# Optimization experiments

Hardware: AMD Instinct MI355X
Metric: run time of the kernel (lower is better)

Reference implementation:

```python
import jax, jax.numpy as jnp
import numpy as np

N, E, G = 50000, 800000, 128
H, NUM_RBF, CUTOFF, TIME_DIM, L = 128, 32, 6.0, 64, 4
MAX_Z, LIGAND_NODE = 128, 1
M_IN = 3 * H + NUM_RBF + 1


def _ln(x, g, b, eps=1e-5):
    mu = x.mean(-1, keepdims=True)
    var = ((x - mu) ** 2).mean(-1, keepdims=True)
    return (x - mu) * jax.lax.rsqrt(var + eps) * g + b


def _sin_emb(t, dim):
    half = dim // 2
    freqs = jnp.exp(jnp.arange(half, dtype=jnp.float32) * (-np.log(10000.0) / (half - 1)))
    args = t[:, None] * freqs[None, :]
    return jnp.concatenate([jnp.sin(args), jnp.cos(args)], axis=-1)


def setup_inputs() -> dict:
    key = jax.random.key(0)
    ks = jax.random.split(key, 32)
    d = {}
    d['z'] = jax.random.randint(ks[0], (N,), 0, MAX_Z)
    d['node_type'] = jax.random.randint(ks[1], (N,), 0, 2)
    d['pos'] = jax.random.normal(ks[2], (N, 3), jnp.float32) * 3.0
    d['edge_index'] = jax.random.randint(ks[3], (2, E), 0, N)
    d['edge_type'] = jax.random.randint(ks[4], (E,), 0, 2)
    d['batch'] = jnp.sort(jax.random.randint(ks[5], (N,), 0, G))
    d['t'] = jax.random.uniform(ks[6], (G,), jnp.float32)

    def lin(k, fi, fo):
        return jax.random.normal(k, (fi, fo), jnp.float32) / np.sqrt(fi)

    d['emb_z'] = jax.random.normal(ks[7], (MAX_Z, H), jnp.float32) * 0.02
    d['emb_nt'] = jax.random.normal(ks[8], (2, H), jnp.float32) * 0.02
    d['in_norm_g'] = jnp.ones((H,), jnp.float32)
    d['in_norm_b'] = jnp.zeros((H,), jnp.float32)
    d['time_w1'] = lin(ks[9], TIME_DIM, H); d['time_b1'] = jnp.zeros((H,), jnp.float32)
    d['time_w2'] = lin(ks[10], H, H); d['time_b2'] = jnp.zeros((H,), jnp.float32)
    d['l_edge_emb'] = jax.random.normal(ks[11], (L, 2, H), jnp.float32) * 0.02
    d['l_msg_w1'] = jax.random.normal(ks[12], (L, M_IN, H), jnp.float32) / np.sqrt(M_IN)
    d['l_msg_b1'] = jnp.zeros((L, H), jnp.float32)
    d['l_msg_w2'] = jax.random.normal(ks[13], (L, H, H), jnp.float32) / np.sqrt(H)
    d['l_msg_b2'] = jnp.zeros((L, H), jnp.float32)
    d['l_upd_w1'] = jax.random.normal(ks[14], (L, 2 * H, H), jnp.float32) / np.sqrt(2 * H)
    d['l_upd_b1'] = jnp.zeros((L, H), jnp.float32)
    d['l_upd_w2'] = jax.random.normal(ks[15], (L, H, H), jnp.float32) / np.sqrt(H)
    d['l_upd_b2'] = jnp.zeros((L, H), jnp.float32)
    d['l_norm_g'] = jnp.ones((L, H), jnp.float32)
    d['l_norm_b'] = jnp.zeros((L, H), jnp.float32)
    d['head_w1'] = lin(ks[16], H, H); d['head_b1'] = jnp.zeros((H,), jnp.float32)
    d['head_w2'] = lin(ks[17], H, 1); d['head_b2'] = jnp.zeros((1,), jnp.float32)
    return d


def reference(z, node_type, pos, edge_index, edge_type, batch, t,
              emb_z, emb_nt, in_norm_g, in_norm_b,
              time_w1, time_b1, time_w2, time_b2,
              l_edge_emb, l_msg_w1, l_msg_b1, l_msg_w2, l_msg_b2,
              l_upd_w1, l_upd_b1, l_upd_w2, l_upd_b2, l_norm_g, l_norm_b,
              head_w1, head_b1, head_w2, head_b2):
    centers = jnp.linspace(0.0, CUTOFF, NUM_RBF)
    step = CUTOFF / (NUM_RBF - 1)
    gamma = 1.0 / max(step * step, 1e-6)

    h = emb_z[jnp.clip(z, 0, MAX_Z - 1)] + emb_nt[node_type]
    tf = jax.nn.silu(_sin_emb(t, TIME_DIM) @ time_w1 + time_b1) @ time_w2 + time_b2
    h = h + tf[batch]
    h = _ln(h, in_norm_g, in_norm_b)

    src, dst = edge_index[0], edge_index[1]
    rel = pos[src] - pos[dst]                     # [E,3]
    dist = jnp.linalg.norm(rel, axis=-1)          # [E]
    radial = jnp.exp(-gamma * (dist[:, None] - centers[None, :]) ** 2)  # [E,R]
    lig = node_type == LIGAND_NODE

    for i in range(L):
        ek = l_edge_emb[i][edge_type]             # [E,H]
        m_in = jnp.concatenate([h[src], h[dst], ek, radial, dist[:, None]], axis=-1)
        msg = jax.nn.silu(m_in @ l_msg_w1[i] + l_msg_b1[i])
        msg = jax.nn.silu(msg @ l_msg_w2[i] + l_msg_b2[i])
        sums = jax.ops.segment_sum(msg, dst, num_segments=N)
        cnt = jax.ops.segment_sum(jnp.ones((E,), h.dtype), dst, num_segments=N)
        agg = sums / jnp.clip(cnt, 1.0)[:, None]
        upd = jax.nn.silu(jnp.concatenate([h, agg], axis=-1) @ l_upd_w1[i] + l_upd_b1[i])
        upd = upd @ l_upd_w2[i] + l_upd_b2[i]
        h = jnp.where(lig[:, None], _ln(h + upd, l_norm_g[i], l_norm_b[i]), h)

    mask = lig.astype(h.dtype)
    gsum = jax.ops.segment_sum(h * mask[:, None], batch, num_segments=G)
    gcnt = jax.ops.segment_sum(mask, batch, num_segments=G)
    gf = gsum / jnp.clip(gcnt, 1.0)[:, None]
    out = jax.nn.silu(gf @ head_w1 + head_b1) @ head_w2 + head_b2
    return out.squeeze(-1)
```

## Files before the change

### kernel.cpp

```cpp
#include <hip/hip_runtime.h>
#include <hip/hip_bf16.h>

#define NN 50000
#define EE 800000
#define GG 128
#define HH 128

typedef __bf16 bf16;
typedef __attribute__((ext_vector_type(8))) __bf16 bf16x8;
typedef __attribute__((ext_vector_type(4))) float f32x4;

__device__ __forceinline__ float silu_f(float x) { return x / (1.0f + __expf(-x)); }

__global__ void prep_weights(const float* __restrict__ w1, const float* __restrict__ w2,
                             const float* __restrict__ u1, const float* __restrict__ u2,
                             const float* __restrict__ ee, const float* __restrict__ mb1,
                             bf16* __restrict__ W1abt, bf16* __restrict__ W1rt,
                             bf16* __restrict__ W2t, bf16* __restrict__ U1t,
                             bf16* __restrict__ U2t) {
    int idx = blockIdx.x * 256 + threadIdx.x;
    if (idx < 131072) {
        int l = idx >> 15, rem = idx & 32767;
        int c = rem >> 7, k = rem & 127;
        int krow = k + ((c >= 128) ? 128 : 0);
        W1abt[idx] = (bf16)w1[(size_t)l * 417 * 128 + (size_t)krow * 128 + (c & 127)];
    } else if ((idx -= 131072) < 32768) {
        int l = idx >> 13, rem = idx & 8191;
        int c = rem >> 6, k = rem & 63;
        const float* w1l = w1 + (size_t)l * 417 * 128;
        float v = 0.0f;
        if (k < 32) v = w1l[(size_t)(384 + k) * 128 + c];
        else if (k == 32) v = w1l[(size_t)416 * 128 + c];
        else if (k == 33) {
            v = mb1[l * 128 + c];
            for (int t = 0; t < 128; ++t)
                v += ee[(size_t)l * 256 + t] * w1l[(size_t)(256 + t) * 128 + c];
        } else if (k == 34) {
            for (int t = 0; t < 128; ++t)
                v += (ee[(size_t)l * 256 + 128 + t] - ee[(size_t)l * 256 + t]) *
                     w1l[(size_t)(256 + t) * 128 + c];
        }
        W1rt[idx] = (bf16)v;
    } else if ((idx -= 32768) < 65536) {
        int l = idx / 16384, rem = idx % 16384;
        int n = rem / 128, k = rem % 128;
        W2t[idx] = (bf16)w2[(size_t)l * 16384 + (size_t)k * 128 + n];
    } else if ((idx -= 65536) < 131072) {
        int l = idx / 32768, rem = idx % 32768;
        int n = rem / 256, k = rem % 256;
        U1t[idx] = (bf16)u1[(size_t)l * 32768 + (size_t)k * 128 + n];
    } else if ((idx -= 131072) < 65536) {
        int l = idx / 16384, rem = idx % 16384;
        int n = rem / 128, k = rem % 128;
        U2t[idx] = (bf16)u2[(size_t)l * 16384 + (size_t)k * 128 + n];
    }
}

__global__ void time_mlp(const float* __restrict__ t, const float* __restrict__ w1,
                         const float* __restrict__ b1, const float* __restrict__ w2,
                         const float* __restrict__ b2, float* __restrict__ tf) {
    int g = blockIdx.x, c = threadIdx.x;
    __shared__ float sL[64], uT[128];
    float tv = t[g];
    if (c < 32) {
        float fr = expf(-(float)c * (logf(10000.0f) / 31.0f));
        float arg = tv * fr;
        sL[c] = sinf(arg);
        sL[c + 32] = cosf(arg);
    }
    __syncthreads();
    float acc = b1[c];
    for (int k = 0; k < 64; ++k) acc += sL[k] * w1[k * 128 + c];
    uT[c] = silu_f(acc);
    __syncthreads();
    float acc2 = b2[c];
    for (int k = 0; k < 128; ++k) acc2 += uT[k] * w2[k * 128 + c];
    tf[g * 128 + c] = acc2;
}

__global__ void node_init(const int* __restrict__ z, const int* __restrict__ nt,
                          const int* __restrict__ batch, const float* __restrict__ tf,
                          const float* __restrict__ emb_z, const float* __restrict__ emb_nt,
                          const float* __restrict__ g, const float* __restrict__ b,
                          float* __restrict__ hg, bf16* __restrict__ hb) {
    int n = blockIdx.x, c = threadIdx.x;
    __shared__ float red[128];
    int zz = min(max(z[n], 0), 127);
    float v = emb_z[zz * 128 + c] + emb_nt[nt[n] * 128 + c] + tf[batch[n] * 128 + c];
    red[c] = v;
    __syncthreads();
    for (int s = 64; s > 0; s >>= 1) { if (c < s) red[c] += red[c + s]; __syncthreads(); }
    float mu = red[0] * (1.0f / 128.0f);
    __syncthreads();
    float dv = v - mu;
    red[c] = dv * dv;
    __syncthreads();
    for (int s = 64; s > 0; s >>= 1) { if (c < s) red[c] += red[c + s]; __syncthreads(); }
    float var = red[0] * (1.0f / 128.0f);
    float o = dv * rsqrtf(var + 1e-5f) * g[c] + b[c];
    hg[(size_t)n * 128 + c] = o;
    hb[(size_t)n * 128 + c] = (bf16)o;
}

__global__ void edge_pre(const int* __restrict__ ei, const float* __restrict__ pos,
                         float* __restrict__ dist_raw, int* __restrict__ cnt) {
    int e = blockIdx.x * 256 + threadIdx.x;
    if (e >= EE) return;
    int s = ei[e], d = ei[EE + e];
    float dx = pos[s * 3 + 0] - pos[d * 3 + 0];
    float dy = pos[s * 3 + 1] - pos[d * 3 + 1];
    float dz = pos[s * 3 + 2] - pos[d * 3 + 2];
    dist_raw[e] = sqrtf(dx * dx + dy * dy + dz * dz);
    atomicAdd(&cnt[d], 1);
}

__global__ void scan_kernel(const int* __restrict__ cnt, int* __restrict__ cursor) {
    __shared__ int part[1024];
    int t = threadIdx.x;
    const int per = (NN + 1023) / 1024;
    int start = t * per, end = min(start + per, NN);
    int s = 0;
    for (int i = start; i < end; ++i) s += cnt[i];
    part[t] = s;
    __syncthreads();
    for (int off = 1; off < 1024; off <<= 1) {
        int v = (t >= off) ? part[t - off] : 0;
        __syncthreads();
        part[t] += v;
        __syncthreads();
    }
    int base = (t == 0) ? 0 : part[t - 1];
    for (int i = start; i < end; ++i) { cursor[i] = base; base += cnt[i]; }
}

__global__ void scatter_kernel(const int* __restrict__ ei, const int* __restrict__ et,
                               const float* __restrict__ dist_raw, int* __restrict__ cursor,
                               int* __restrict__ src_s, int* __restrict__ dst_s,
                               int* __restrict__ type_s, float* __restrict__ dist_s) {
    int e = blockIdx.x * 256 + threadIdx.x;
    if (e >= EE) return;
    int d = ei[EE + e];
    int p = atomicAdd(&cursor[d], 1);
    src_s[p] = ei[e];
    dst_s[p] = d;
    type_s[p] = et[e];
    dist_s[p] = dist_raw[e];
}

__global__ __launch_bounds__(256) void node_pre(
    const bf16* __restrict__ hb, const bf16* __restrict__ W1abt,
    bf16* __restrict__ Xsb, bf16* __restrict__ Xdb) {
    __shared__ bf16 xL[64 * 128];
    const int tid = threadIdx.x;
    const int lane = tid & 63, wave = tid >> 6;
    const int wr = wave >> 1, wc = wave & 1;
    const int lrow = lane & 15, lgrp = lane >> 4;
    const int nb0 = blockIdx.x * 64;
    const int r0 = wr * 32 + lrow, r1 = r0 + 16;

    for (int i = tid; i < 64 * 16; i += 256) {
        const int row = i >> 4, cc = i & 15;
        const int node = nb0 + row;
        bf16x8 v;
        if (node < NN) v = *(const bf16x8*)(hb + (size_t)node * 128 + cc * 8);
        else { for (int j = 0; j < 8; ++j) v[j] = (bf16)0.0f; }
        *(bf16x8*)(xL + row * 128 + ((cc ^ (row & 15)) * 8)) = v;
    }
    __syncthreads();

    f32x4 acc[2][8] = {};
    for (int ks = 0; ks < 4; ++ks) {
        const int cb = ks * 4 + lgrp;
        bf16x8 a0 = *(const bf16x8*)(xL + r0 * 128 + ((cb ^ (r0 & 15)) * 8));
        bf16x8 a1 = *(const bf16x8*)(xL + r1 * 128 + ((cb ^ (r1 & 15)) * 8));
        const int k0 = ks * 32 + lgrp * 8;
#pragma unroll
        for (int ni = 0; ni < 8; ++ni) {
            const int col = wc * 128 + ni * 16 + lrow;
            bf16x8 b = *(const bf16x8*)(W1abt + (size_t)col * 128 + k0);
            acc[0][ni] = __builtin_amdgcn_mfma_f32_16x16x32_bf16(a0, b, acc[0][ni], 0, 0, 0);
            acc[1][ni] = __builtin_amdgcn_mfma_f32_16x16x32_bf16(a1, b, acc[1][ni], 0, 0, 0);
        }
    }
#pragma unroll
    for (int mi = 0; mi < 2; ++mi) {
#pragma unroll
        for (int r = 0; r < 4; ++r) {
            const int row = wr * 32 + mi * 16 + lgrp * 4 + r;
            const int node = nb0 + row;
            if (node >= NN) continue;
#pragma unroll
            for (int ni = 0; ni < 8; ++ni) {
                const int col = wc * 128 + ni * 16 + lrow;
                float v = (mi == 0 ? acc[0][ni][r] : acc[1][ni][r]);
                if (col < 128) Xsb[(size_t)node * 128 + col] = (bf16)v;
                else Xdb[(size_t)node * 128 + (col - 128)] = (bf16)v;
            }
        }
    }
}

__global__ __launch_bounds__(256) void edge_kernel(
    const int* __restrict__ src_s, const int* __restrict__ dst_s,
    const int* __restrict__ type_s, const float* __restrict__ dist_s,
    const bf16* __restrict__ Xsb, const bf16* __restrict__ Xdb,
    const bf16* __restrict__ W1rt, const bf16* __restrict__ W2t,
    const float* __restrict__ b2, float* __restrict__ sums) {
    __shared__ bf16 xsL[64 * 128];
    __shared__ bf16 xdL[64 * 128];
    __shared__ int dstL[64];
    __shared__ int srcL[64];
    const int tid = threadIdx.x;
    const int lane = tid & 63, wave = tid >> 6;
    const int wr = wave >> 1, wc = wave & 1;
    const int lrow = lane & 15, lgrp = lane >> 4;
    const int eb = blockIdx.x * 64;

    const int r0 = wr * 32 + lrow;
    const int r1 = r0 + 16;
    const int e0 = eb + r0, e1 = eb + r1;
    const int ty0 = type_s[e0], ty1 = type_s[e1];
    const float di0 = dist_s[e0], di1 = dist_s[e1];
    if (tid < 64) { dstL[tid] = dst_s[eb + tid]; srcL[tid] = src_s[eb + tid]; }
    __syncthreads();

#pragma unroll
    for (int it = 0; it < 4; ++it) {
        const int ci = tid + it * 256;
        const int row = ci >> 4, cc = ci & 15;
        const int ccs = (cc ^ (row & 15)) << 3;
        bf16x8 vs = *(const bf16x8*)(Xsb + (size_t)srcL[row] * 128 + ccs);
        bf16x8 vd = *(const bf16x8*)(Xdb + (size_t)dstL[row] * 128 + ccs);
        *(bf16x8*)(xsL + ci * 8) = vs;
        *(bf16x8*)(xdL + ci * 8) = vd;
    }

    const float step = 6.0f / 31.0f;
    const float gamma = 1.0f / (step * step);

    f32x4 acc[2][4] = {};
#pragma unroll
    for (int ks = 0; ks < 2; ++ks) {
        const int k0 = ks * 32 + lgrp * 8;
        bf16x8 a0, a1;
        if (k0 < 32) {
#pragma unroll
            for (int j = 0; j < 8; ++j) {
                float cj = (float)(k0 + j) * step;
                float v0 = di0 - cj, v1 = di1 - cj;
                a0[j] = (bf16)__expf(-gamma * v0 * v0);
                a1[j] = (bf16)__expf(-gamma * v1 * v1);
            }
        } else {
#pragma unroll
            for (int j = 0; j < 8; ++j) { a0[j] = (bf16)0.0f; a1[j] = (bf16)0.0f; }
            if (k0 == 32) {
                a0[0] = (bf16)di0; a1[0] = (bf16)di1;
                a0[1] = (bf16)1.0f; a1[1] = (bf16)1.0f;
                a0[2] = (bf16)(float)ty0; a1[2] = (bf16)(float)ty1;
            }
        }
#pragma unroll
        for (int ni = 0; ni < 4; ++ni) {
            const int col = wc * 64 + ni * 16 + lrow;
            bf16x8 b = *(const bf16x8*)(W1rt + (size_t)col * 64 + k0);
            acc[0][ni] = __builtin_amdgcn_mfma_f32_16x16x32_bf16(a0, b, acc[0][ni], 0, 0, 0);
            acc[1][ni] = __builtin_amdgcn_mfma_f32_16x16x32_bf16(a1, b, acc[1][ni], 0, 0, 0);
        }
    }
    __syncthreads();

#pragma unroll
    for (int mi = 0; mi < 2; ++mi) {
#pragma unroll
        for (int r = 0; r < 4; ++r) {
            const int row = wr * 32 + mi * 16 + lgrp * 4 + r;
            const int base = row * 128, sw = row & 15;
#pragma unroll
            for (int ni = 0; ni < 4; ++ni) {
                const int col = wc * 64 + ni * 16 + lrow;
                const int idx = base + (((col >> 3) ^ sw) << 3) + (col & 7);
                float v = (mi == 0 ? acc[0][ni][r] : acc[1][ni][r]) +
                          (float)xsL[idx] + (float)xdL[idx];
                if (mi == 0) acc[0][ni][r] = silu_f(v);
                else acc[1][ni][r] = silu_f(v);
            }
        }
    }
    __syncthreads();

#pragma unroll
    for (int mi = 0; mi < 2; ++mi) {
#pragma unroll
        for (int r = 0; r < 4; ++r) {
            const int row = wr * 32 + mi * 16 + lgrp * 4 + r;
            const int base = row * 128, sw = row & 15;
#pragma unroll
            for (int ni = 0; ni < 4; ++ni) {
                const int col = wc * 64 + ni * 16 + lrow;
                const int idx = base + (((col >> 3) ^ sw) << 3) + (col & 7);
                xsL[idx] = (bf16)(mi == 0 ? acc[0][ni][r] : acc[1][ni][r]);
            }
        }
    }
    __syncthreads();

    f32x4 acc2[2][4] = {};
#pragma unroll
    for (int ks = 0; ks < 4; ++ks) {
        const int cb = ks * 4 + lgrp;
        bf16x8 a0 = *(const bf16x8*)(xsL + r0 * 128 + ((cb ^ (r0 & 15)) * 8));
        bf16x8 a1 = *(const bf16x8*)(xsL + r1 * 128 + ((cb ^ (r1 & 15)) * 8));
        const int k0 = ks * 32 + lgrp * 8;
#pragma unroll
        for (int ni = 0; ni < 4; ++ni) {
            const int col = wc * 64 + ni * 16 + lrow;
            bf16x8 b = *(const bf16x8*)(W2t + (size_t)col * 128 + k0);
            acc2[0][ni] = __builtin_amdgcn_mfma_f32_16x16x32_bf16(a0, b, acc2[0][ni], 0, 0, 0);
            acc2[1][ni] = __builtin_amdgcn_mfma_f32_16x16x32_bf16(a1, b, acc2[1][ni], 0, 0, 0);
        }
    }
#pragma unroll
    for (int mi = 0; mi < 2; ++mi) {
#pragma unroll
        for (int ni = 0; ni < 4; ++ni) {
            const int col = wc * 64 + ni * 16 + lrow;
            const float bias = b2[col];
#pragma unroll
            for (int r = 0; r < 4; ++r) {
                const int row = wr * 32 + mi * 16 + lgrp * 4 + r;
                float v = silu_f((mi == 0 ? acc2[0][ni][r] : acc2[1][ni][r]) + bias);
                xdL[row * 128 + col] = (bf16)v;
            }
        }
    }
    __syncthreads();
    {
        const int cp = (tid & 63) * 2;
        const int q = tid >> 6;
        float a0s = 0.0f, a1s = 0.0f;
        int cur = dstL[q * 16];
        for (int i = 0; i < 16; ++i) {
            const int row = q * 16 + i;
            const int dd = dstL[row];
            if (dd != cur) {
                atomicAdd(&sums[(size_t)cur * 128 + cp], a0s);
                atomicAdd(&sums[(size_t)cur * 128 + cp + 1], a1s);
                a0s = 0.0f; a1s = 0.0f; cur = dd;
            }
            const unsigned u = *(const unsigned*)(xdL + row * 128 + cp);
            a0s += __uint_as_float(u << 16);
            a1s += __uint_as_float(u & 0xffff0000u);
        }
        atomicAdd(&sums[(size_t)cur * 128 + cp], a0s);
        atomicAdd(&sums[(size_t)cur * 128 + cp + 1], a1s);
    }
}

__global__ __launch_bounds__(256) void node_kernel(
    float* __restrict__ hg, bf16* __restrict__ hb, float* __restrict__ sums,
    const int* __restrict__ cnt, const int* __restrict__ node_type,
    const bf16* __restrict__ U1t, const bf16* __restrict__ U2t,
    const float* __restrict__ ub1, const float* __restrict__ ub2,
    const float* __restrict__ ng, const float* __restrict__ nb_) {
    __shared__ char smem[49152];
    bf16* xL = (bf16*)smem;
    bf16* uL = (bf16*)(smem + 32768);
    float* u2f = (float*)smem;
    const int tid = threadIdx.x;
    const int lane = tid & 63, wave = tid >> 6;
    const int wr = wave >> 1, wc = wave & 1;
    const int lrow = lane & 15, lgrp = lane >> 4;
    const int nb0 = blockIdx.x * 64;
    const int r0 = wr * 32 + lrow, r1 = r0 + 16;

    for (int i = tid; i < 64 * 32; i += 256) {
        const int row = i >> 5, cc = i & 31;
        const int node = nb0 + row;
        bf16x8 v;
        if (node < NN) {
            const int col8 = cc * 8;
            if (col8 < 128) {
                v = *(const bf16x8*)(hb + (size_t)node * 128 + col8);
            } else {
                const float inv = 1.0f / fmaxf((float)cnt[node], 1.0f);
                float4* p0 = (float4*)(sums + (size_t)node * 128 + (col8 - 128));
                float4* p1 = (float4*)(sums + (size_t)node * 128 + (col8 - 128) + 4);
                const float4 f0 = *p0;
                const float4 f1 = *p1;
                v[0] = (bf16)(f0.x * inv); v[1] = (bf16)(f0.y * inv);
                v[2] = (bf16)(f0.z * inv); v[3] = (bf16)(f0.w * inv);
                v[4] = (bf16)(f1.x * inv); v[5] = (bf16)(f1.y * inv);
                v[6] = (bf16)(f1.z * inv); v[7] = (bf16)(f1.w * inv);
                *p0 = make_float4(0.f, 0.f, 0.f, 0.f);
                *p1 = make_float4(0.f, 0.f, 0.f, 0.f);
            }
        } else {
#pragma unroll
            for (int j = 0; j < 8; ++j) v[j] = (bf16)0.0f;
        }
        *(bf16x8*)(xL + row * 256 + ((cc ^ (row & 15)) * 8)) = v;
    }
    __syncthreads();

    f32x4 acc[2][4] = {};
    for (int ks = 0; ks < 8; ++ks) {
        const int cb = ks * 4 + lgrp;
        bf16x8 a0 = *(const bf16x8*)(xL + r0 * 256 + ((cb ^ (r0 & 15)) * 8));
        bf16x8 a1 = *(const bf16x8*)(xL + r1 * 256 + ((cb ^ (r1 & 15)) * 8));
        const int k0 = ks * 32 + lgrp * 8;
#pragma unroll
        for (int ni = 0; ni < 4; ++ni) {
            const int col = wc * 64 + ni * 16 + lrow;
            bf16x8 b = *(const bf16x8*)(U1t + (size_t)col * 256 + k0);
            acc[0][ni] = __builtin_amdgcn_mfma_f32_16x16x32_bf16(a0, b, acc[0][ni], 0, 0, 0);
            acc[1][ni] = __builtin_amdgcn_mfma_f32_16x16x32_bf16(a1, b, acc[1][ni], 0, 0, 0);
        }
    }
#pragma unroll
    for (int mi = 0; mi < 2; ++mi) {
#pragma unroll
        for (int ni = 0; ni < 4; ++ni) {
            const int col = wc * 64 + ni * 16 + lrow;
            const float bias = ub1[col];
            const int cc = col >> 3;
#pragma unroll
            for (int r = 0; r < 4; ++r) {
                const int row = wr * 32 + mi * 16 + lgrp * 4 + r;
                float v = silu_f((mi == 0 ? acc[0][ni][r] : acc[1][ni][r]) + bias);
                uL[row * 128 + ((cc ^ (row & 15)) * 8) + (col & 7)] = (bf16)v;
            }
        }
    }
    __syncthreads();

    f32x4 acc2[2][4] = {};
    for (int ks = 0; ks < 4; ++ks) {
        const int cb = ks * 4 + lgrp;
        bf16x8 a0 = *(const bf16x8*)(uL + r0 * 128 + ((cb ^ (r0 & 15)) * 8));
        bf16x8 a1 = *(const bf16x8*)(uL + r1 * 128 + ((cb ^ (r1 & 15)) * 8));
        const int k0 = ks * 32 + lgrp * 8;
#pragma unroll
        for (int ni = 0; ni < 4; ++ni) {
            const int col = wc * 64 + ni * 16 + lrow;
            bf16x8 b = *(const bf16x8*)(U2t + (size_t)col * 128 + k0);
            acc2[0][ni] = __builtin_amdgcn_mfma_f32_16x16x32_bf16(a0, b, acc2[0][ni], 0, 0, 0);
            acc2[1][ni] = __builtin_amdgcn_mfma_f32_16x16x32_bf16(a1, b, acc2[1][ni], 0, 0, 0);
        }
    }
    __syncthreads();
#pragma unroll
    for (int mi = 0; mi < 2; ++mi) {
#pragma unroll
        for (int ni = 0; ni < 4; ++ni) {
            const int col = wc * 64 + ni * 16 + lrow;
            const float bias = ub2[col];
#pragma unroll
            for (int r = 0; r < 4; ++r) {
                const int row = wr * 32 + mi * 16 + lgrp * 4 + r;
                u2f[row * 129 + col] = (mi == 0 ? acc2[0][ni][r] : acc2[1][ni][r]) + bias;
            }
        }
    }
    __syncthreads();
    {
        const int row = tid >> 2, sl = tid & 3;
        const int node = nb0 + row;
        const bool lig = (node < NN) && (node_type[node] == 1);
        float sum = 0.0f, sq = 0.0f;
        if (lig) {
#pragma unroll
            for (int k = 0; k < 32; ++k) {
                const int c = sl + (k << 2);
                float s = hg[(size_t)node * 128 + c] + u2f[row * 129 + c];
                u2f[row * 129 + c] = s;
                sum += s; sq += s * s;
            }
        }
        sum += __shfl_xor(sum, 1); sq += __shfl_xor(sq, 1);
        sum += __shfl_xor(sum, 2); sq += __shfl_xor(sq, 2);
        if (lig) {
            const float mu = sum * (1.0f / 128.0f);
            const float var = sq * (1.0f / 128.0f) - mu * mu;
            const float rstd = rsqrtf(var + 1e-5f);
#pragma unroll
            for (int k = 0; k < 32; ++k) {
                const int c = sl + (k << 2);
                float s = u2f[row * 129 + c];
                float o = (s - mu) * rstd * ng[c] + nb_[c];
                hg[(size_t)node * 128 + c] = o;
                hb[(size_t)node * 128 + c] = (bf16)o;
            }
        }
    }
}

__global__ void pool_kernel(const int* __restrict__ nt, const int* __restrict__ batch,
                            const float* __restrict__ hg, float* __restrict__ gsum,
                            float* __restrict__ gcnt) {
    int idx = blockIdx.x * 256 + threadIdx.x;
    int n = idx >> 7, c = idx & 127;
    if (n >= NN) return;
    if (nt[n] == 1) {
        int b = batch[n];
        atomicAdd(&gsum[b * 128 + c], hg[(size_t)n * 128 + c]);
        if (c == 0) atomicAdd(&gcnt[b], 1.0f);
    }
}

__global__ void head_kernel(const float* __restrict__ gsum, const float* __restrict__ gcnt,
                            const float* __restrict__ w1, const float* __restrict__ b1,
                            const float* __restrict__ w2, const float* __restrict__ b2,
                            float* __restrict__ out) {
    int g = blockIdx.x, c = threadIdx.x;
    __shared__ float gfL[128], uH[128];
    float inv = 1.0f / fmaxf(gcnt[g], 1.0f);
    gfL[c] = gsum[g * 128 + c] * inv;
    __syncthreads();
    float acc = b1[c];
    for (int k = 0; k < 128; ++k) acc += gfL[k] * w1[k * 128 + c];
    uH[c] = silu_f(acc);
    __syncthreads();
    gfL[c] = uH[c] * w2[c];
    __syncthreads();
    for (int s = 64; s > 0; s >>= 1) { if (c < s) gfL[c] += gfL[c + s]; __syncthreads(); }
    if (c == 0) out[g] = gfL[0] + b2[0];
}

extern "C" void kernel_launch(void* const* d_in, const int* in_sizes, int n_in,
                              void* d_out, int out_size, void* d_ws, size_t ws_size,
                              hipStream_t stream) {
    const int* z = (const int*)d_in[0];
    const int* node_type = (const int*)d_in[1];
    const float* pos = (const float*)d_in[2];
    const int* edge_index = (const int*)d_in[3];
    const int* edge_type = (const int*)d_in[4];
    const int* batch = (const int*)d_in[5];
    const float* t_in = (const float*)d_in[6];
    const float* emb_z = (const float*)d_in[7];
    const float* emb_nt = (const float*)d_in[8];
    const float* in_norm_g = (const float*)d_in[9];
    const float* in_norm_b = (const float*)d_in[10];
    const float* time_w1 = (const float*)d_in[11];
    const float* time_b1 = (const float*)d_in[12];
    const float* time_w2 = (const float*)d_in[13];
    const float* time_b2 = (const float*)d_in[14];
    const float* l_edge_emb = (const float*)d_in[15];
    const float* l_msg_w1 = (const float*)d_in[16];
    const float* l_msg_b1 = (const float*)d_in[17];
    const float* l_msg_w2 = (const float*)d_in[18];
    const float* l_msg_b2 = (const float*)d_in[19];
    const float* l_upd_w1 = (const float*)d_in[20];
    const float* l_upd_b1 = (const float*)d_in[21];
    const float* l_upd_w2 = (const float*)d_in[22];
    const float* l_upd_b2 = (const float*)d_in[23];
    const float* l_norm_g = (const float*)d_in[24];
    const float* l_norm_b = (const float*)d_in[25];
    const float* head_w1 = (const float*)d_in[26];
    const float* head_b1 = (const float*)d_in[27];
    const float* head_w2 = (const float*)d_in[28];
    const float* head_b2 = (const float*)d_in[29];
    float* out = (float*)d_out;

    char* w = (char*)d_ws;
    auto alloc = [&](size_t bytes) {
        char* p = w;
        w += (bytes + 255) & ~(size_t)255;
        return p;
    };
    float* hg = (float*)alloc((size_t)NN * 128 * 4);
    bf16* hb = (bf16*)alloc((size_t)NN * 128 * 2);
    float* sums = (float*)alloc((size_t)NN * 128 * 4);
    bf16* Xsb = (bf16*)alloc((size_t)NN * 128 * 2);
    bf16* Xdb = (bf16*)alloc((size_t)NN * 128 * 2);
    int* cnt = (int*)alloc((size_t)NN * 4);
    int* cursor = (int*)alloc((size_t)NN * 4);
    int* src_s = (int*)alloc((size_t)EE * 4);
    int* dst_s = (int*)alloc((size_t)EE * 4);
    int* type_s = (int*)alloc((size_t)EE * 4);
    float* dist_s = (float*)alloc((size_t)EE * 4);
    float* dist_raw = (float*)alloc((size_t)EE * 4);
    bf16* W1abt = (bf16*)alloc((size_t)4 * 256 * 128 * 2);
    bf16* W1rt = (bf16*)alloc((size_t)4 * 128 * 64 * 2);
    bf16* W2t = (bf16*)alloc((size_t)4 * 128 * 128 * 2);
    bf16* U1t = (bf16*)alloc((size_t)4 * 128 * 256 * 2);
    bf16* U2t = (bf16*)alloc((size_t)4 * 128 * 128 * 2);
    float* tf = (float*)alloc((size_t)GG * 128 * 4);
    float* gsum = (float*)alloc((size_t)GG * 128 * 4);
    float* gcnt = (float*)alloc((size_t)GG * 4);

    hipMemsetAsync(cnt, 0, (size_t)NN * 4, stream);
    hipMemsetAsync(sums, 0, (size_t)NN * 128 * 4, stream);
    prep_weights<<<1664, 256, 0, stream>>>(l_msg_w1, l_msg_w2, l_upd_w1, l_upd_w2,
                                           l_edge_emb, l_msg_b1, W1abt, W1rt, W2t, U1t, U2t);
    time_mlp<<<GG, 128, 0, stream>>>(t_in, time_w1, time_b1, time_w2, time_b2, tf);
    node_init<<<NN, 128, 0, stream>>>(z, node_type, batch, tf, emb_z, emb_nt,
                                      in_norm_g, in_norm_b, hg, hb);
    edge_pre<<<(EE + 255) / 256, 256, 0, stream>>>(edge_index, pos, dist_raw, cnt);
    scan_kernel<<<1, 1024, 0, stream>>>(cnt, cursor);
    scatter_kernel<<<(EE + 255) / 256, 256, 0, stream>>>(edge_index, edge_type, dist_raw,
                                                         cursor, src_s, dst_s, type_s, dist_s);
    for (int l = 0; l < 4; ++l) {
        node_pre<<<(NN + 63) / 64, 256, 0, stream>>>(hb, W1abt + (size_t)l * 32768, Xsb, Xdb);
        edge_kernel<<<EE / 64, 256, 0, stream>>>(
            src_s, dst_s, type_s, dist_s, Xsb, Xdb, W1rt + (size_t)l * 8192,
            W2t + (size_t)l * 16384, l_msg_b2 + l * 128, sums);
        node_kernel<<<(NN + 63) / 64, 256, 0, stream>>>(
            hg, hb, sums, cnt, node_type, U1t + (size_t)l * 32768, U2t + (size_t)l * 16384,
            l_upd_b1 + l * 128, l_upd_b2 + l * 128, l_norm_g + l * 128, l_norm_b + l * 128);
    }
    hipMemsetAsync(gsum, 0, (size_t)GG * 128 * 4, stream);
    hipMemsetAsync(gcnt, 0, (size_t)GG * 4, stream);
    pool_kernel<<<(NN * 128 + 255) / 256, 256, 0, stream>>>(node_type, batch, hg, gsum, gcnt);
    head_kernel<<<GG, 128, 0, stream>>>(gsum, gcnt, head_w1, head_b1, head_w2, head_b2, out);
}
```

Measured before the change: 1.603 ms.

## Transpose edge MFMA operands and gather node features directly into registers

Swaps the MFMA operand roles so weights are the A operand and per-edge activations the B operand, which puts each lane's outputs along contiguous columns of one edge. With that layout, the src/dst node feature rows are read from global memory straight into registers as 4-wide vectors instead of being staged through two shared-memory tiles. This removes one LDS buffer and several barriers, and uses a padded stride for the final message tile. In exchange the global gathers become smaller 8-byte accesses issued after the first GEMM rather than overlapped with it.

Result: no change. 1.629 ms (+1.6%).

```diff
diff --git a/kernel.cpp b/kernel.cpp
--- a/kernel.cpp
+++ b/kernel.cpp
@@ -5,9 +5,11 @@
 #define EE 800000
 #define GG 128
 #define HH 128
+#define MP 136
 
 typedef __bf16 bf16;
 typedef __attribute__((ext_vector_type(8))) __bf16 bf16x8;
+typedef __attribute__((ext_vector_type(4))) __bf16 bf16x4;
 typedef __attribute__((ext_vector_type(4))) float f32x4;
 
 __device__ __forceinline__ float silu_f(float x) { return x / (1.0f + __expf(-x)); }
@@ -206,135 +208,128 @@
     const bf16* __restrict__ Xsb, const bf16* __restrict__ Xdb,
     const bf16* __restrict__ W1rt, const bf16* __restrict__ W2t,
     const float* __restrict__ b2, float* __restrict__ sums) {
-    __shared__ bf16 xsL[64 * 128];
-    __shared__ bf16 xdL[64 * 128];
-    __shared__ int dstL[64];
-    __shared__ int srcL[64];
+    __shared__ bf16 mL[64 * MP];
+    __shared__ int srcL[64], dstL[64], typeL[64];
+    __shared__ float distL[64];
     const int tid = threadIdx.x;
     const int lane = tid & 63, wave = tid >> 6;
-    const int wr = wave >> 1, wc = wave & 1;
-    const int lrow = lane & 15, lgrp = lane >> 4;
+    const int wh = wave >> 1, wc = wave & 1;
+    const int e15 = lane & 15, lgrp = lane >> 4;
     const int eb = blockIdx.x * 64;
 
-    const int r0 = wr * 32 + lrow;
-    const int r1 = r0 + 16;
-    const int e0 = eb + r0, e1 = eb + r1;
-    const int ty0 = type_s[e0], ty1 = type_s[e1];
-    const float di0 = dist_s[e0], di1 = dist_s[e1];
-    if (tid < 64) { dstL[tid] = dst_s[eb + tid]; srcL[tid] = src_s[eb + tid]; }
-    __syncthreads();
-
-#pragma unroll
-    for (int it = 0; it < 4; ++it) {
-        const int ci = tid + it * 256;
-        const int row = ci >> 4, cc = ci & 15;
-        const int ccs = (cc ^ (row & 15)) << 3;
-        bf16x8 vs = *(const bf16x8*)(Xsb + (size_t)srcL[row] * 128 + ccs);
-        bf16x8 vd = *(const bf16x8*)(Xdb + (size_t)dstL[row] * 128 + ccs);
-        *(bf16x8*)(xsL + ci * 8) = vs;
-        *(bf16x8*)(xdL + ci * 8) = vd;
-    }
+    if (tid < 64) {
+        srcL[tid] = src_s[eb + tid];
+        dstL[tid] = dst_s[eb + tid];
+        typeL[tid] = type_s[eb + tid];
+        distL[tid] = dist_s[eb + tid];
+    }
+    __syncthreads();
+
+    const int el0 = wh * 32 + e15, el1 = el0 + 16;
+    const float d0 = distL[el0], d1 = distL[el1];
+    const float t0 = (float)typeL[el0], t1 = (float)typeL[el1];
 
     const float step = 6.0f / 31.0f;
     const float gamma = 1.0f / (step * step);
 
     f32x4 acc[2][4] = {};
-#pragma unroll
-    for (int ks = 0; ks < 2; ++ks) {
+    {
+        bf16x8 b0, b1;
+#pragma unroll
+        for (int j = 0; j < 8; ++j) {
+            float cj = (float)(lgrp * 8 + j) * step;
+            float v0 = d0 - cj, v1 = d1 - cj;
+            b0[j] = (bf16)__expf(-gamma * v0 * v0);
+            b1[j] = (bf16)__expf(-gamma * v1 * v1);
+        }
+#pragma unroll
+        for (int ct = 0; ct < 4; ++ct) {
+            const int col = wc * 64 + ct * 16 + e15;
+            bf16x8 a = *(const bf16x8*)(W1rt + (size_t)col * 64 + lgrp * 8);
+            acc[0][ct] = __builtin_amdgcn_mfma_f32_16x16x32_bf16(a, b0, acc[0][ct], 0, 0, 0);
+            acc[1][ct] = __builtin_amdgcn_mfma_f32_16x16x32_bf16(a, b1, acc[1][ct], 0, 0, 0);
+        }
+    }
+    {
+        bf16x8 b0, b1;
+#pragma unroll
+        for (int j = 0; j < 8; ++j) { b0[j] = (bf16)0.0f; b1[j] = (bf16)0.0f; }
+        if (lgrp == 0) {
+            b0[0] = (bf16)d0; b1[0] = (bf16)d1;
+            b0[1] = (bf16)1.0f; b1[1] = (bf16)1.0f;
+            b0[2] = (bf16)t0; b1[2] = (bf16)t1;
+        }
+#pragma unroll
+        for (int ct = 0; ct < 4; ++ct) {
+            const int col = wc * 64 + ct * 16 + e15;
+            bf16x8 a = *(const bf16x8*)(W1rt + (size_t)col * 64 + 32 + lgrp * 8);
+            acc[0][ct] = __builtin_amdgcn_mfma_f32_16x16x32_bf16(a, b0, acc[0][ct], 0, 0, 0);
+            acc[1][ct] = __builtin_amdgcn_mfma_f32_16x16x32_bf16(a, b1, acc[1][ct], 0, 0, 0);
+        }
+    }
+
+#pragma unroll
+    for (int et = 0; et < 2; ++et) {
+        const int eloc = wh * 32 + et * 16 + e15;
+        const bf16* xsp = Xsb + (size_t)srcL[eloc] * 128;
+        const bf16* xdp = Xdb + (size_t)dstL[eloc] * 128;
+        bf16x4 xs[4], xd[4];
+#pragma unroll
+        for (int ct = 0; ct < 4; ++ct) {
+            const int col0 = wc * 64 + ct * 16 + lgrp * 4;
+            xs[ct] = *(const bf16x4*)(xsp + col0);
+            xd[ct] = *(const bf16x4*)(xdp + col0);
+        }
+#pragma unroll
+        for (int ct = 0; ct < 4; ++ct) {
+            const int col0 = wc * 64 + ct * 16 + lgrp * 4;
+            bf16x4 pk;
+#pragma unroll
+            for (int r = 0; r < 4; ++r) {
+                float v = (et == 0 ? acc[0][ct][r] : acc[1][ct][r]) +
+                          (float)xs[ct][r] + (float)xd[ct][r];
+                pk[r] = (bf16)silu_f(v);
+            }
+            const int cc = col0 >> 3;
+            *(bf16x4*)(mL + eloc * 128 + ((cc ^ (eloc & 15)) << 3) + (col0 & 7)) = pk;
+        }
+    }
+    __syncthreads();
+
+    f32x4 acc2[2][4] = {};
+#pragma unroll
+    for (int ks = 0; ks < 4; ++ks) {
         const int k0 = ks * 32 + lgrp * 8;
-        bf16x8 a0, a1;
-        if (k0 < 32) {
-#pragma unroll
-            for (int j = 0; j < 8; ++j) {
-                float cj = (float)(k0 + j) * step;
-                float v0 = di0 - cj, v1 = di1 - cj;
-                a0[j] = (bf16)__expf(-gamma * v0 * v0);
-                a1[j] = (bf16)__expf(-gamma * v1 * v1);
-            }
-        } else {
-#pragma unroll
-            for (int j = 0; j < 8; ++j) { a0[j] = (bf16)0.0f; a1[j] = (bf16)0.0f; }
-            if (k0 == 32) {
-                a0[0] = (bf16)di0; a1[0] = (bf16)di1;
-                a0[1] = (bf16)1.0f; a1[1] = (bf16)1.0f;
-                a0[2] = (bf16)(float)ty0; a1[2] = (bf16)(float)ty1;
-            }
-        }
-#pragma unroll
-        for (int ni = 0; ni < 4; ++ni) {
-            const int col = wc * 64 + ni * 16 + lrow;
-            bf16x8 b = *(const bf16x8*)(W1rt + (size_t)col * 64 + k0);
-            acc[0][ni] = __builtin_amdgcn_mfma_f32_16x16x32_bf16(a0, b, acc[0][ni], 0, 0, 0);
-            acc[1][ni] = __builtin_amdgcn_mfma_f32_16x16x32_bf16(a1, b, acc[1][ni], 0, 0, 0);
-        }
-    }
-    __syncthreads();
-
-#pragma unroll
-    for (int mi = 0; mi < 2; ++mi) {
-#pragma unroll
-        for (int r = 0; r < 4; ++r) {
-            const int row = wr * 32 + mi * 16 + lgrp * 4 + r;
-            const int base = row * 128, sw = row & 15;
-#pragma unroll
-            for (int ni = 0; ni < 4; ++ni) {
-                const int col = wc * 64 + ni * 16 + lrow;
-                const int idx = base + (((col >> 3) ^ sw) << 3) + (col & 7);
-                float v = (mi == 0 ? acc[0][ni][r] : acc[1][ni][r]) +
-                          (float)xsL[idx] + (float)xdL[idx];
-                if (mi == 0) acc[0][ni][r] = silu_f(v);
-                else acc[1][ni][r] = silu_f(v);
-            }
-        }
-    }
-    __syncthreads();
-
-#pragma unroll
-    for (int mi = 0; mi < 2; ++mi) {
-#pragma unroll
-        for (int r = 0; r < 4; ++r) {
-            const int row = wr * 32 + mi * 16 + lgrp * 4 + r;
-            const int base = row * 128, sw = row & 15;
-#pragma unroll
-            for (int ni = 0; ni < 4; ++ni) {
-                const int col = wc * 64 + ni * 16 + lrow;
-                const int idx = base + (((col >> 3) ^ sw) << 3) + (col & 7);
-                xsL[idx] = (bf16)(mi == 0 ? acc[0][ni][r] : acc[1][ni][r]);
-            }
-        }
-    }
-    __syncthreads();
-
-    f32x4 acc2[2][4] = {};
-#pragma unroll
-    for (int ks = 0; ks < 4; ++ks) {
-        const int cb = ks * 4 + lgrp;
-        bf16x8 a0 = *(const bf16x8*)(xsL + r0 * 128 + ((cb ^ (r0 & 15)) * 8));
-        bf16x8 a1 = *(const bf16x8*)(xsL + r1 * 128 + ((cb ^ (r1 & 15)) * 8));
-        const int k0 = ks * 32 + lgrp * 8;
-#pragma unroll
-        for (int ni = 0; ni < 4; ++ni) {
-            const int col = wc * 64 + ni * 16 + lrow;
-            bf16x8 b = *(const bf16x8*)(W2t + (size_t)col * 128 + k0);
-            acc2[0][ni] = __builtin_amdgcn_mfma_f32_16x16x32_bf16(a0, b, acc2[0][ni], 0, 0, 0);
-            acc2[1][ni] = __builtin_amdgcn_mfma_f32_16x16x32_bf16(a1, b, acc2[1][ni], 0, 0, 0);
-        }
-    }
-#pragma unroll
-    for (int mi = 0; mi < 2; ++mi) {
-#pragma unroll
-        for (int ni = 0; ni < 4; ++ni) {
-            const int col = wc * 64 + ni * 16 + lrow;
-            const float bias = b2[col];
-#pragma unroll
-            for (int r = 0; r < 4; ++r) {
-                const int row = wr * 32 + mi * 16 + lgrp * 4 + r;
-                float v = silu_f((mi == 0 ? acc2[0][ni][r] : acc2[1][ni][r]) + bias);
-                xdL[row * 128 + col] = (bf16)v;
-            }
-        }
-    }
-    __syncthreads();
+        const int kc = k0 >> 3;
+        bf16x8 b0 = *(const bf16x8*)(mL + el0 * 128 + ((kc ^ (el0 & 15)) << 3));
+        bf16x8 b1 = *(const bf16x8*)(mL + el1 * 128 + ((kc ^ (el1 & 15)) << 3));
+#pragma unroll
+        for (int ct = 0; ct < 4; ++ct) {
+            const int c2 = wc * 64 + ct * 16 + e15;
+            bf16x8 a = *(const bf16x8*)(W2t + (size_t)c2 * 128 + k0);
+            acc2[0][ct] = __builtin_amdgcn_mfma_f32_16x16x32_bf16(a, b0, acc2[0][ct], 0, 0, 0);
+            acc2[1][ct] = __builtin_amdgcn_mfma_f32_16x16x32_bf16(a, b1, acc2[1][ct], 0, 0, 0);
+        }
+    }
+    __syncthreads();
+
+#pragma unroll
+    for (int et = 0; et < 2; ++et) {
+        const int eloc = wh * 32 + et * 16 + e15;
+#pragma unroll
+        for (int ct = 0; ct < 4; ++ct) {
+            const int col0 = wc * 64 + ct * 16 + lgrp * 4;
+            const float4 bb = *(const float4*)(b2 + col0);
+            bf16x4 pk;
+            pk[0] = (bf16)silu_f((et == 0 ? acc2[0][ct][0] : acc2[1][ct][0]) + bb.x);
+            pk[1] = (bf16)silu_f((et == 0 ? acc2[0][ct][1] : acc2[1][ct][1]) + bb.y);
+            pk[2] = (bf16)silu_f((et == 0 ? acc2[0][ct][2] : acc2[1][ct][2]) + bb.z);
+            pk[3] = (bf16)silu_f((et == 0 ? acc2[0][ct][3] : acc2[1][ct][3]) + bb.w);
+            *(bf16x4*)(mL + eloc * MP + col0) = pk;
+        }
+    }
+    __syncthreads();
+
     {
         const int cp = (tid & 63) * 2;
         const int q = tid >> 6;
@@ -348,7 +343,7 @@
                 atomicAdd(&sums[(size_t)cur * 128 + cp + 1], a1s);
                 a0s = 0.0f; a1s = 0.0f; cur = dd;
             }
-            const unsigned u = *(const unsigned*)(xdL + row * 128 + cp);
+            const unsigned u = *(const unsigned*)(mL + row * MP + cp);
             a0s += __uint_as_float(u << 16);
             a1s += __uint_as_float(u & 0xffff0000u);
         }
```

## Fuse next-layer node projection into node kernel and pre-sum gathered features

Applied to the files above, without the earlier changes.

The per-layer node_pre launch is folded into the tail of node_kernel, which now stages the updated bf16 node features in shared memory and computes the next layer's source/destination projections with MFMA. This removes one launch and a re-read of hb per layer. The edge kernel also adds the gathered Xs and Xd rows once while loading, storing a single padded buffer and writing silu output straight to a separate message buffer, which drops one shared-memory pass and a barrier. The trade-offs are an extra bf16 rounding of the summed projections and more shared memory and registers in node_kernel.

Result: faster. 1.387 ms (-13.5%).

```diff
diff --git a/kernel.cpp b/kernel.cpp
--- a/kernel.cpp
+++ b/kernel.cpp
@@ -5,6 +5,7 @@
 #define EE 800000
 #define GG 128
 #define HH 128
+#define XPB 136
 
 typedef __bf16 bf16;
 typedef __attribute__((ext_vector_type(8))) __bf16 bf16x8;
@@ -206,8 +207,8 @@
     const bf16* __restrict__ Xsb, const bf16* __restrict__ Xdb,
     const bf16* __restrict__ W1rt, const bf16* __restrict__ W2t,
     const float* __restrict__ b2, float* __restrict__ sums) {
-    __shared__ bf16 xsL[64 * 128];
-    __shared__ bf16 xdL[64 * 128];
+    __shared__ bf16 xbL[64 * XPB];
+    __shared__ bf16 msgL[64 * 128];
     __shared__ int dstL[64];
     __shared__ int srcL[64];
     const int tid = threadIdx.x;
@@ -225,14 +226,14 @@
     __syncthreads();
 
 #pragma unroll
-    for (int it = 0; it < 4; ++it) {
-        const int ci = tid + it * 256;
-        const int row = ci >> 4, cc = ci & 15;
-        const int ccs = (cc ^ (row & 15)) << 3;
-        bf16x8 vs = *(const bf16x8*)(Xsb + (size_t)srcL[row] * 128 + ccs);
-        bf16x8 vd = *(const bf16x8*)(Xdb + (size_t)dstL[row] * 128 + ccs);
-        *(bf16x8*)(xsL + ci * 8) = vs;
-        *(bf16x8*)(xdL + ci * 8) = vd;
+    for (int i = tid; i < 64 * 16; i += 256) {
+        const int row = i >> 4, c8 = (i & 15) << 3;
+        bf16x8 a = *(const bf16x8*)(Xsb + (size_t)srcL[row] * 128 + c8);
+        bf16x8 b = *(const bf16x8*)(Xdb + (size_t)dstL[row] * 128 + c8);
+        bf16x8 s;
+#pragma unroll
+        for (int j = 0; j < 8; ++j) s[j] = (bf16)((float)a[j] + (float)b[j]);
+        *(bf16x8*)(xbL + row * XPB + c8) = s;
     }
 
     const float step = 6.0f / 31.0f;
@@ -275,31 +276,14 @@
 #pragma unroll
         for (int r = 0; r < 4; ++r) {
             const int row = wr * 32 + mi * 16 + lgrp * 4 + r;
-            const int base = row * 128, sw = row & 15;
+            const bf16* xr = xbL + row * XPB;
 #pragma unroll
             for (int ni = 0; ni < 4; ++ni) {
                 const int col = wc * 64 + ni * 16 + lrow;
-                const int idx = base + (((col >> 3) ^ sw) << 3) + (col & 7);
-                float v = (mi == 0 ? acc[0][ni][r] : acc[1][ni][r]) +
-                          (float)xsL[idx] + (float)xdL[idx];
-                if (mi == 0) acc[0][ni][r] = silu_f(v);
-                else acc[1][ni][r] = silu_f(v);
-            }
-        }
-    }
-    __syncthreads();
-
-#pragma unroll
-    for (int mi = 0; mi < 2; ++mi) {
-#pragma unroll
-        for (int r = 0; r < 4; ++r) {
-            const int row = wr * 32 + mi * 16 + lgrp * 4 + r;
-            const int base = row * 128, sw = row & 15;
-#pragma unroll
-            for (int ni = 0; ni < 4; ++ni) {
-                const int col = wc * 64 + ni * 16 + lrow;
-                const int idx = base + (((col >> 3) ^ sw) << 3) + (col & 7);
-                xsL[idx] = (bf16)(mi == 0 ? acc[0][ni][r] : acc[1][ni][r]);
+                float v = (mi == 0 ? acc[0][ni][r] : acc[1][ni][r]) + (float)xr[col];
+                v = silu_f(v);
+                const int cc = col >> 3;
+                msgL[row * 128 + ((cc ^ (row & 15)) * 8) + (col & 7)] = (bf16)v;
             }
         }
     }
@@ -309,8 +293,8 @@
 #pragma unroll
     for (int ks = 0; ks < 4; ++ks) {
         const int cb = ks * 4 + lgrp;
-        bf16x8 a0 = *(const bf16x8*)(xsL + r0 * 128 + ((cb ^ (r0 & 15)) * 8));
-        bf16x8 a1 = *(const bf16x8*)(xsL + r1 * 128 + ((cb ^ (r1 & 15)) * 8));
+        bf16x8 a0 = *(const bf16x8*)(msgL + r0 * 128 + ((cb ^ (r0 & 15)) * 8));
+        bf16x8 a1 = *(const bf16x8*)(msgL + r1 * 128 + ((cb ^ (r1 & 15)) * 8));
         const int k0 = ks * 32 + lgrp * 8;
 #pragma unroll
         for (int ni = 0; ni < 4; ++ni) {
@@ -330,7 +314,7 @@
             for (int r = 0; r < 4; ++r) {
                 const int row = wr * 32 + mi * 16 + lgrp * 4 + r;
                 float v = silu_f((mi == 0 ? acc2[0][ni][r] : acc2[1][ni][r]) + bias);
-                xdL[row * 128 + col] = (bf16)v;
+                xbL[row * XPB + col] = (bf16)v;
             }
         }
     }
@@ -348,7 +332,7 @@
                 atomicAdd(&sums[(size_t)cur * 128 + cp + 1], a1s);
                 a0s = 0.0f; a1s = 0.0f; cur = dd;
             }
-            const unsigned u = *(const unsigned*)(xdL + row * 128 + cp);
+            const unsigned u = *(const unsigned*)(xbL + row * XPB + cp);
             a0s += __uint_as_float(u << 16);
             a1s += __uint_as_float(u & 0xffff0000u);
         }
@@ -362,11 +346,14 @@
     const int* __restrict__ cnt, const int* __restrict__ node_type,
     const bf16* __restrict__ U1t, const bf16* __restrict__ U2t,
     const float* __restrict__ ub1, const float* __restrict__ ub2,
-    const float* __restrict__ ng, const float* __restrict__ nb_) {
-    __shared__ char smem[49152];
+    const float* __restrict__ ng, const float* __restrict__ nb_,
+    const bf16* __restrict__ W1abt_next, bf16* __restrict__ Xsb,
+    bf16* __restrict__ Xdb, int compute_x) {
+    __shared__ char smem[49664];
     bf16* xL = (bf16*)smem;
     bf16* uL = (bf16*)(smem + 32768);
-    float* u2f = (float*)smem;
+    bf16* hnL = (bf16*)smem;
+    float* u2f = (float*)(smem + 16384);
     const int tid = threadIdx.x;
     const int lane = tid & 63, wave = tid >> 6;
     const int wr = wave >> 1, wc = wave & 1;
@@ -449,6 +436,7 @@
         }
     }
     __syncthreads();
+
 #pragma unroll
     for (int mi = 0; mi < 2; ++mi) {
 #pragma unroll
@@ -462,7 +450,16 @@
             }
         }
     }
-    __syncthreads();
+    for (int i = tid; i < 64 * 16; i += 256) {
+        const int row = i >> 4, cc = i & 15;
+        const int node = nb0 + row;
+        bf16x8 v;
+        if (node < NN) v = *(const bf16x8*)(hb + (size_t)node * 128 + cc * 8);
+        else { for (int j = 0; j < 8; ++j) v[j] = (bf16)0.0f; }
+        *(bf16x8*)(hnL + row * 128 + ((cc ^ (row & 15)) * 8)) = v;
+    }
+    __syncthreads();
+
     {
         const int row = tid >> 2, sl = tid & 3;
         const int node = nb0 + row;
@@ -490,6 +487,41 @@
                 float o = (s - mu) * rstd * ng[c] + nb_[c];
                 hg[(size_t)node * 128 + c] = o;
                 hb[(size_t)node * 128 + c] = (bf16)o;
+                const int cc = c >> 3;
+                hnL[row * 128 + ((cc ^ (row & 15)) << 3) + (c & 7)] = (bf16)o;
+            }
+        }
+    }
+    if (!compute_x) return;
+    __syncthreads();
+
+    f32x4 accX[2][8] = {};
+    for (int ks = 0; ks < 4; ++ks) {
+        const int cb = ks * 4 + lgrp;
+        bf16x8 a0 = *(const bf16x8*)(hnL + r0 * 128 + ((cb ^ (r0 & 15)) * 8));
+        bf16x8 a1 = *(const bf16x8*)(hnL + r1 * 128 + ((cb ^ (r1 & 15)) * 8));
+        const int k0 = ks * 32 + lgrp * 8;
+#pragma unroll
+        for (int ni = 0; ni < 8; ++ni) {
+            const int col = wc * 128 + ni * 16 + lrow;
+            bf16x8 b = *(const bf16x8*)(W1abt_next + (size_t)col * 128 + k0);
+            accX[0][ni] = __builtin_amdgcn_mfma_f32_16x16x32_bf16(a0, b, accX[0][ni], 0, 0, 0);
+            accX[1][ni] = __builtin_amdgcn_mfma_f32_16x16x32_bf16(a1, b, accX[1][ni], 0, 0, 0);
+        }
+    }
+#pragma unroll
+    for (int mi = 0; mi < 2; ++mi) {
+#pragma unroll
+        for (int r = 0; r < 4; ++r) {
+            const int row = wr * 32 + mi * 16 + lgrp * 4 + r;
+            const int node = nb0 + row;
+            if (node >= NN) continue;
+#pragma unroll
+            for (int ni = 0; ni < 8; ++ni) {
+                const int col = wc * 128 + ni * 16 + lrow;
+                float v = (mi == 0 ? accX[0][ni][r] : accX[1][ni][r]);
+                if (col < 128) Xsb[(size_t)node * 128 + col] = (bf16)v;
+                else Xdb[(size_t)node * 128 + (col - 128)] = (bf16)v;
             }
         }
     }
@@ -600,14 +632,16 @@
     scan_kernel<<<1, 1024, 0, stream>>>(cnt, cursor);
     scatter_kernel<<<(EE + 255) / 256, 256, 0, stream>>>(edge_index, edge_type, dist_raw,
                                                          cursor, src_s, dst_s, type_s, dist_s);
+    node_pre<<<(NN + 63) / 64, 256, 0, stream>>>(hb, W1abt, Xsb, Xdb);
     for (int l = 0; l < 4; ++l) {
-        node_pre<<<(NN + 63) / 64, 256, 0, stream>>>(hb, W1abt + (size_t)l * 32768, Xsb, Xdb);
         edge_kernel<<<EE / 64, 256, 0, stream>>>(
             src_s, dst_s, type_s, dist_s, Xsb, Xdb, W1rt + (size_t)l * 8192,
             W2t + (size_t)l * 16384, l_msg_b2 + l * 128, sums);
+        const int nl = (l < 3) ? (l + 1) : 0;
         node_kernel<<<(NN + 63) / 64, 256, 0, stream>>>(
             hg, hb, sums, cnt, node_type, U1t + (size_t)l * 32768, U2t + (size_t)l * 16384,
-            l_upd_b1 + l * 128, l_upd_b2 + l * 128, l_norm_g + l * 128, l_norm_b + l * 128);
+            l_upd_b1 + l * 128, l_upd_b2 + l * 128, l_norm_g + l * 128, l_norm_b + l * 128,
+            W1abt + (size_t)nl * 32768, Xsb, Xdb, (l < 3) ? 1 : 0);
     }
     hipMemsetAsync(gsum, 0, (size_t)GG * 128 * 4, stream);
     hipMemsetAsync(gcnt, 0, (size_t)GG * 4, stream);
```
